# Optimization experiments

Measured on AMD Instinct MI355X. Metric: run time of the kernel, lower is better.

Reference implementation:

```python
import jax, jax.numpy as jnp
import numpy as np

B, T, D, C = 16, 2048, 512, 20
K_EASY, K_HARD = 40, 20
M_BIG, M_SMALL = 7, 3
A4 = A5 = A6 = A7 = 1.0
EPS = 1e-05
DROP_P = 0.6


def setup_inputs() -> dict:
    key = jax.random.key(0)
    ks = jax.random.split(key, 6)
    attn = jax.random.uniform(ks[0], (B, T, 1), dtype=jnp.float32)
    mu = jax.random.normal(ks[1], (B, T, D), dtype=jnp.float32)
    var = jax.random.uniform(ks[2], (B, T, D), dtype=jnp.float32) * 0.9 + 0.1
    mu_clip = jax.random.normal(ks[3], (B, T, D), dtype=jnp.float32)
    text_feat = jax.random.normal(ks[4], (C, D), dtype=jnp.float32)
    keep = (jax.random.uniform(ks[5], (B, T)) >= DROP_P).astype(jnp.float32)
    drop_mask = keep / (1.0 - DROP_P)  # inverted-dropout mask on a ones tensor
    return dict(attn=attn, mu=mu, var=var, mu_clip=mu_clip, text_feat=text_feat, drop_mask=drop_mask)


def _normalize(x, axis=-1):
    n = jnp.linalg.norm(x, axis=axis, keepdims=True)
    return x / jnp.maximum(n, 1e-12)


def _select_topk(scores, emb, k):
    # torch: sort desc, take first k indices, gather along time dim
    _, idx = jax.lax.top_k(scores, k)  # [B,k]
    return jnp.take_along_axis(emb, idx[:, :, None], axis=1)  # [B,k,D]


def _window_reduce(x, w, op_min):
    # binary erosion/dilation along time with structure ones((1,w)), border_value=0
    lo, hi = w // 2, w - 1 - w // 2
    xp = jnp.pad(x, ((0, 0), (lo, hi)), constant_values=0.0)
    if op_min:
        return jax.lax.reduce_window(xp, jnp.inf, jax.lax.min, (1, w), (1, 1), 'VALID')
    return jax.lax.reduce_window(xp, -jnp.inf, jax.lax.max, (1, w), (1, 1), 'VALID')


def _kl_distance(mu_p, cov_p, mu_q, cov_q):
    # vectorized over all (i in k_p) x (j in k_q) pairs
    cov_p = cov_p + EPS
    cov_q = cov_q + EPS
    d = mu_p.shape[-1]
    diff = mu_q[:, None, :, :] - mu_p[:, :, None, :]        # [B,kp,kq,D]
    term1 = 0.5 * jnp.sum(diff * diff / cov_q[:, None, :, :], axis=-1)
    term2 = 0.5 * (jnp.sum(jnp.log(cov_q), -1)[:, None, :] - jnp.sum(jnp.log(cov_p), -1)[:, :, None])
    term3 = 0.5 * jnp.sum(cov_p[:, :, None, :] / cov_q[:, None, :, :], axis=-1)
    dist = term1 + term2 + term3 - 0.5 * d
    return jnp.mean(1.0 / (dist + 1.0), axis=(1, 2))        # [B]


def _prob_contrastive(hard_q, easy_pos, easy_neg):
    pos = _kl_distance(hard_q[0], hard_q[1], easy_pos[0], easy_pos[1])
    neg = _kl_distance(hard_q[0], hard_q[1], easy_neg[0], easy_neg[1])
    return jnp.mean(-(jnp.log(pos) + jnp.log(1.0 - neg)))


def _forward(attn, mu, var, mu_clip, text_feat, drop_mask):
    a = attn[..., 0]                                        # [B,T]
    a_drop = a * drop_mask
    a_rev = jnp.max(a, axis=1, keepdims=True) - a
    a_rev_drop = a_rev * drop_mask
    easy_act = (_select_topk(a_drop, mu, K_EASY), _select_topk(a_drop, var, K_EASY))
    easy_bkg = (_select_topk(a_rev_drop, mu, K_EASY), _select_topk(a_rev_drop, var, K_EASY))

    med = jnp.median(a, axis=1, keepdims=True)
    abin = jnp.where(a > med, 1.0, 0.0)
    er_M = _window_reduce(abin, M_BIG, True)
    er_m = _window_reduce(abin, M_SMALL, True)
    inner = jax.lax.stop_gradient(er_m - er_M)              # mask computed on detached numpy in torch
    dl_m = _window_reduce(abin, M_SMALL, False)
    dl_M = _window_reduce(abin, M_BIG, False)
    outer = jax.lax.stop_gradient(dl_M - dl_m)
    a_inner = a * inner
    a_outer = a * outer
    hard_act = (_select_topk(a_inner, mu, K_HARD), _select_topk(a_inner, var, K_HARD))
    hard_bkg = (_select_topk(a_outer, mu, K_HARD), _select_topk(a_outer, var, K_HARD))

    # Distillation
    sim = jnp.einsum('btd,btd->bt', _normalize(mu), _normalize(mu_clip))
    distill = A4 * (-jnp.log(jnp.mean((sim + 1.0) / 2.0)))

    act_loss = A5 * _prob_contrastive(hard_act, easy_act, easy_bkg)
    bkg_loss = A6 * _prob_contrastive(hard_bkg, easy_bkg, easy_act)

    emb = _normalize(text_feat)
    sim_m = emb @ jax.lax.stop_gradient(emb.T) - jnp.eye(emb.shape[0], dtype=emb.dtype)
    ortho = A7 * jnp.linalg.norm(sim_m)

    total = distill + act_loss + bkg_loss + ortho
    return total, distill, act_loss, bkg_loss, ortho


def reference(attn, mu, var, mu_clip, text_feat, drop_mask):
    return _forward(attn, mu, var, mu_clip, text_feat, drop_mask)
```

## Files before the change

kernel.cpp:

```cpp
#include <hip/hip_runtime.h>
#include <math.h>


#define BB 16
#define TT 2048
#define DD 512
#define CC 20
#define KEASY 40
#define KHARD 20
#define EPSF 1e-5f

typedef unsigned long long u64;

template <int CTRL>
__device__ __forceinline__ float dpp_mov(float x) {
  return __int_as_float(__builtin_amdgcn_update_dpp(
      0, __float_as_int(x), CTRL, 0xF, 0xF, true));
}
template <int CTRL, int RM>
__device__ __forceinline__ unsigned dpp_movu(unsigned x) {
  return (unsigned)__builtin_amdgcn_update_dpp(0, (int)x, CTRL, RM, 0xF, true);
}
__device__ __forceinline__ float wsum63(float v) {
  v += dpp_mov<0x111>(v);
  v += dpp_mov<0x112>(v);
  v += dpp_mov<0x114>(v);
  v += dpp_mov<0x118>(v);
  v += dpp_mov<0x142>(v);
  v += dpp_mov<0x143>(v);
  return v;
}
__device__ __forceinline__ float wsum_bc(float v) {
  return __int_as_float(__builtin_amdgcn_readlane(__float_as_int(wsum63(v)), 63));
}
__device__ __forceinline__ float wmax63(float v) {
  v = fmaxf(v, dpp_mov<0x111>(v));
  v = fmaxf(v, dpp_mov<0x112>(v));
  v = fmaxf(v, dpp_mov<0x114>(v));
  v = fmaxf(v, dpp_mov<0x118>(v));
  v = fmaxf(v, dpp_mov<0x142>(v));
  v = fmaxf(v, dpp_mov<0x143>(v));
  return v;
}
__device__ __forceinline__ unsigned wscanu(unsigned v) {
  v += dpp_movu<0x111, 0xF>(v);
  v += dpp_movu<0x112, 0xF>(v);
  v += dpp_movu<0x114, 0xF>(v);
  v += dpp_movu<0x118, 0xF>(v);
  v += dpp_movu<0x142, 0xa>(v);
  v += dpp_movu<0x143, 0xc>(v);
  return v;
}

__device__ __forceinline__ float radix_kth(const float* sbuf, unsigned k,
                                           unsigned* s_hist4, unsigned* s_state,
                                           int tid, int wid) {
#pragma unroll 1
  for (int round = 0; round < 4; ++round) {
    s_hist4[tid] = 0;
    s_hist4[256 + tid] = 0;
    s_hist4[512 + tid] = 0;
    s_hist4[768 + tid] = 0;
    if (round == 0 && tid == 0) { s_state[0] = 0u; s_state[1] = k; }
    __syncthreads();
    const int shift = 24 - 8 * round;
    const unsigned mask_hi = (round == 0) ? 0u : (0xFFFFFFFFu << (shift + 8));
    const unsigned pref = s_state[0];
    const unsigned kk = s_state[1];
    unsigned* myhist = s_hist4 + (wid << 8);
    unsigned curbin = 0xFFFFFFFFu, curc = 0;
    for (int i = tid; i < TT; i += 256) {
      const unsigned key = __float_as_uint(sbuf[i]);
      if ((key & mask_hi) == pref) {
        const unsigned bin = 255u - ((key >> shift) & 255u);
        if (bin == curbin) {
          curc++;
        } else {
          if (curc) atomicAdd(&myhist[curbin], curc);
          curbin = bin;
          curc = 1;
        }
      }
    }
    if (curc) atomicAdd(&myhist[curbin], curc);
    __syncthreads();
    if (tid < 64) {
      const uint4 h0 = *(const uint4*)(s_hist4 + 4 * tid);
      const uint4 h1 = *(const uint4*)(s_hist4 + 256 + 4 * tid);
      const uint4 h2 = *(const uint4*)(s_hist4 + 512 + 4 * tid);
      const uint4 h3 = *(const uint4*)(s_hist4 + 768 + 4 * tid);
      const unsigned b0 = h0.x + h1.x + h2.x + h3.x;
      const unsigned b1 = h0.y + h1.y + h2.y + h3.y;
      const unsigned b2 = h0.z + h1.z + h2.z + h3.z;
      const unsigned b3 = h0.w + h1.w + h2.w + h3.w;
      const unsigned s0 = b0, s1 = s0 + b1, s2 = s1 + b2, s3 = s2 + b3;
      const unsigned P = wscanu(s3);
      const unsigned E = P - s3;
      const u64 bal = __ballot(P >= kk);
      const int L = (int)__ffsll(bal) - 1;
      if (tid == L) {
        unsigned binj, cb;
        if (E + s0 >= kk)      { binj = 0u; cb = E; }
        else if (E + s1 >= kk) { binj = 1u; cb = E + s0; }
        else if (E + s2 >= kk) { binj = 2u; cb = E + s1; }
        else                   { binj = 3u; cb = E + s2; }
        const unsigned digit = 255u - (4u * (unsigned)tid + binj);
        s_state[0] = pref | (digit << shift);
        s_state[1] = kk - cb;
      }
    }
    __syncthreads();
  }
  return __uint_as_float(s_state[0]);
}

__global__ __launch_bounds__(256, 2) void k_main1(const float* __restrict__ attn,
                                                  const float* __restrict__ drop,
                                                  const float* __restrict__ mu,
                                                  const float* __restrict__ muc,
                                                  const float* __restrict__ var,
                                                  int* __restrict__ idxb,
                                                  float* __restrict__ slogb,
                                                  float* __restrict__ part) {
  const int tid = threadIdx.x, wid = tid >> 6, lane = tid & 63;

  if (blockIdx.x >= 64) {
    __shared__ float s_red[4];
    const int d = blockIdx.x - 64;
    const int row0 = d * 16 + wid * 4;
    const float* pmu = mu + (size_t)row0 * DD + lane * 4;
    const float* pmc = muc + (size_t)row0 * DD + lane * 4;
    float4 x[8], y[8];
#pragma unroll
    for (int r = 0; r < 4; r++) {
      const int off = r * DD;
      x[2 * r]     = *(const float4*)(pmu + off);
      x[2 * r + 1] = *(const float4*)(pmu + off + 256);
      y[2 * r]     = *(const float4*)(pmc + off);
      y[2 * r + 1] = *(const float4*)(pmc + off + 256);
    }
    float wacc = 0.f;
#pragma unroll
    for (int r = 0; r < 4; r++) {
      const float4 cxa = x[2 * r], cxb = x[2 * r + 1];
      const float4 cya = y[2 * r], cyb = y[2 * r + 1];
      float dot = 0.f, n1 = 0.f, n2 = 0.f;
      dot = fmaf(cxa.x, cya.x, fmaf(cxa.y, cya.y, fmaf(cxa.z, cya.z, fmaf(cxa.w, cya.w, dot))));
      n1 = fmaf(cxa.x, cxa.x, fmaf(cxa.y, cxa.y, fmaf(cxa.z, cxa.z, fmaf(cxa.w, cxa.w, n1))));
      n2 = fmaf(cya.x, cya.x, fmaf(cya.y, cya.y, fmaf(cya.z, cya.z, fmaf(cya.w, cya.w, n2))));
      dot = fmaf(cxb.x, cyb.x, fmaf(cxb.y, cyb.y, fmaf(cxb.z, cyb.z, fmaf(cxb.w, cyb.w, dot))));
      n1 = fmaf(cxb.x, cxb.x, fmaf(cxb.y, cxb.y, fmaf(cxb.z, cxb.z, fmaf(cxb.w, cxb.w, n1))));
      n2 = fmaf(cyb.x, cyb.x, fmaf(cyb.y, cyb.y, fmaf(cyb.z, cyb.z, fmaf(cyb.w, cyb.w, n2))));
      dot = wsum63(dot);
      n1 = wsum63(n1);
      n2 = wsum63(n2);
      if (lane == 63) {
        const float sim = dot / (fmaxf(sqrtf(n1), 1e-12f) * fmaxf(sqrtf(n2), 1e-12f));
        wacc += (sim + 1.0f) * 0.5f;
      }
    }
    if (lane == 63) s_red[wid] = wacc;
    __syncthreads();
    if (tid == 0) part[d] = s_red[0] + s_red[1] + s_red[2] + s_red[3];
    return;
  }

  __shared__ float s_a[TT];
  __shared__ float s_v[TT];
  __shared__ __align__(16) unsigned s_hist4[1024];
  __shared__ unsigned s_state[2];
  __shared__ float s_bc[4];
  __shared__ unsigned s_bcu[4];
  __shared__ int s_idx[KEASY];

  const int b = blockIdx.x >> 2, sel = blockIdx.x & 3;
  for (int i = tid; i < TT; i += 256) s_a[i] = attn[b * TT + i];
  __syncthreads();

  float med = 0.f, mx = 0.f;
  if (sel == 1) {
    float lm = 0.f;
    for (int i = tid; i < TT; i += 256) lm = fmaxf(lm, s_a[i]);
    lm = wmax63(lm);
    if (lane == 63) s_bc[wid] = lm;
    __syncthreads();
    mx = fmaxf(fmaxf(s_bc[0], s_bc[1]), fmaxf(s_bc[2], s_bc[3]));
  } else if (sel >= 2) {
    const float v1 = radix_kth(s_a, 1024u, s_hist4, s_state, tid, wid);
    unsigned c = 0;
    float m2 = 0.f;
    for (int i = tid; i < TT; i += 256) {
      const float x = s_a[i];
      c += (x >= v1) ? 1u : 0u;
      m2 = (x < v1) ? fmaxf(m2, x) : m2;
    }
    c = wscanu(c);
    m2 = wmax63(m2);
    if (lane == 63) { s_bc[wid] = m2; s_bcu[wid] = c; }
    __syncthreads();
    const unsigned ctot = s_bcu[0] + s_bcu[1] + s_bcu[2] + s_bcu[3];
    const float m2t = fmaxf(fmaxf(s_bc[0], s_bc[1]), fmaxf(s_bc[2], s_bc[3]));
    const float v2 = (ctot >= 1025u) ? v1 : m2t;
    med = 0.5f * (v1 + v2);
  }

  for (int i = tid; i < TT; i += 256) {
    const float a = s_a[i];
    float score;
    if (sel == 0) {
      score = a * drop[b * TT + i];
    } else if (sel == 1) {
      score = (mx - a) * drop[b * TT + i];
    } else {
      bool sall = true, ball = true, sany = false, bany = false;
#pragma unroll
      for (int o = -3; o <= 3; o++) {
        const int t = i + o;
        const bool one = (t >= 0 && t < TT) ? (s_a[t] > med) : false;
        if (o >= -1 && o <= 1) { sall = sall && one; sany = sany || one; }
        ball = ball && one;
        bany = bany || one;
      }
      score = (sel == 2) ? ((sall && !ball) ? a : 0.f)
                         : ((bany && !sany) ? a : 0.f);
    }
    s_v[i] = score;
  }
  const unsigned K = (sel < 2) ? KEASY : KHARD;
  const float thr = radix_kth(s_v, K, s_hist4, s_state, tid, wid);

  if (tid < 64) {
    float v[32];
#pragma unroll
    for (int r = 0; r < 32; r++) v[r] = s_v[r * 64 + lane];
    unsigned cgt = 0;
#pragma unroll
    for (int r = 0; r < 32; r++) cgt += (unsigned)__popcll(__ballot(v[r] > thr));
    unsigned need = (cgt < K) ? (K - cgt) : 0u;
    unsigned base = 0;
    const u64 lmask = (1ull << lane) - 1;
    int* dst = idxb + sel * (BB * KEASY) + b * KEASY;
#pragma unroll
    for (int r = 0; r < 32; r++) {
      const bool gt = v[r] > thr;
      const bool eq = v[r] == thr;
      const u64 beq = __ballot(eq);
      const unsigned neq = (unsigned)__popcll(beq);
      const unsigned take = (need < neq) ? need : neq;
      const bool tk = eq && ((unsigned)__popcll(beq & lmask) < take);
      const u64 bsel = __ballot(gt || tk);
      if (gt || tk) {
        const unsigned pos = base + (unsigned)__popcll(bsel & lmask);
        if (pos < K) {
          dst[pos] = r * 64 + lane;
          s_idx[pos] = r * 64 + lane;
        }
      }
      base += (unsigned)__popcll(bsel);
      need -= take;
    }
  }
  __syncthreads();

  const int Ksel = (sel < 2) ? KEASY : KHARD;
  for (int j = wid; j < Ksel; j += 4) {
    const int t = s_idx[j];
    const float* row = var + ((size_t)b * TT + t) * DD;
    float a2 = 0.f;
#pragma unroll
    for (int c = 0; c < 2; c++) {
      float4 vv = *(const float4*)(row + c * 256 + lane * 4);
      a2 += __logf(vv.x + EPSF) + __logf(vv.y + EPSF) +
            __logf(vv.z + EPSF) + __logf(vv.w + EPSF);
    }
    a2 = wsum63(a2);
    if (lane == 63) slogb[sel * 640 + b * 40 + j] = a2;
  }
}

__global__ __launch_bounds__(256, 1) void k_part2(const float* __restrict__ mu,
                                                  const float* __restrict__ var,
                                                  const int* __restrict__ idxb,
                                                  const float* __restrict__ slogb,
                                                  const float* __restrict__ text,
                                                  double* __restrict__ acc) {
  __shared__ __align__(16) float smem[2 * KHARD * DD];
  const int tid = threadIdx.x, wid = tid >> 6, lane = tid & 63;
  const int blk = blockIdx.x;

  if (blk < 256) {
    const int b = blk >> 4, klid = (blk >> 2) & 3, qc = blk & 3;
    const int psel = (klid < 2) ? 2 : 3;
    const int qsel = (klid == 0 || klid == 3) ? 0 : 1;
    float* sP1 = smem;
    float* sP2 = smem + KHARD * DD;
    __shared__ float sSlogP[KHARD];
    __shared__ float s_out[4];
    if (tid < KHARD) sSlogP[tid] = slogb[psel * 640 + b * 40 + tid];
    for (int i = tid; i < KHARD * 128; i += 256) {
      const int p = i >> 7, c = (i & 127) * 4;
      const int t = idxb[psel * 640 + b * 40 + p];
      const size_t base = ((size_t)b * TT + t) * DD + c;
      const float4 m = *(const float4*)(mu + base);
      const float4 vv = *(const float4*)(var + base);
      float4 p1;
      p1.x = fmaf(m.x, m.x, vv.x + EPSF);
      p1.y = fmaf(m.y, m.y, vv.y + EPSF);
      p1.z = fmaf(m.z, m.z, vv.z + EPSF);
      p1.w = fmaf(m.w, m.w, vv.w + EPSF);
      *(float4*)(sP1 + p * DD + c) = p1;
      *(float4*)(sP2 + p * DD + c) = m;
    }
    __syncthreads();

    const int d0 = lane * 4, d1 = 256 + lane * 4;
    const int qbase_i = qsel * 640 + b * 40 + qc * 10;
    float wacc = 0.f;
#pragma unroll 1
    for (int j = wid; j < 10; j += 4) {
      const int qidx = idxb[qbase_i + j];
      const float cslq = slogb[qbase_i + j];
      const float* qm = mu + ((size_t)b * TT + qidx) * DD;
      const float* qv = var + ((size_t)b * TT + qidx) * DD;
      const float4 cma = *(const float4*)(qm + d0);
      const float4 cmb = *(const float4*)(qm + d1);
      const float4 cva = *(const float4*)(qv + d0);
      const float4 cvb = *(const float4*)(qv + d1);
      float4 ra, rb, qra, qrb;
      ra.x = 1.0f / (cva.x + EPSF); ra.y = 1.0f / (cva.y + EPSF);
      ra.z = 1.0f / (cva.z + EPSF); ra.w = 1.0f / (cva.w + EPSF);
      rb.x = 1.0f / (cvb.x + EPSF); rb.y = 1.0f / (cvb.y + EPSF);
      rb.z = 1.0f / (cvb.z + EPSF); rb.w = 1.0f / (cvb.w + EPSF);
      qra.x = cma.x * ra.x; qra.y = cma.y * ra.y;
      qra.z = cma.z * ra.z; qra.w = cma.w * ra.w;
      qrb.x = cmb.x * rb.x; qrb.y = cmb.y * rb.y;
      qrb.z = cmb.z * rb.z; qrb.w = cmb.w * rb.w;
      float cqp = cma.x * qra.x + cma.y * qra.y + cma.z * qra.z + cma.w * qra.w +
                  cmb.x * qrb.x + cmb.y * qrb.y + cmb.z * qrb.z + cmb.w * qrb.w;
      const float cq = wsum63(cqp);
      for (int p = 0; p < KHARD; p++) {
        const float4 p1a = *(const float4*)(sP1 + p * DD + d0);
        const float4 p1b = *(const float4*)(sP1 + p * DD + d1);
        const float4 p2a = *(const float4*)(sP2 + p * DD + d0);
        const float4 p2b = *(const float4*)(sP2 + p * DD + d1);
        const float s1 = p1a.x * ra.x + p1a.y * ra.y + p1a.z * ra.z + p1a.w * ra.w +
                         p1b.x * rb.x + p1b.y * rb.y + p1b.z * rb.z + p1b.w * rb.w;
        const float s2 = p2a.x * qra.x + p2a.y * qra.y + p2a.z * qra.z + p2a.w * qra.w +
                         p2b.x * qrb.x + p2b.y * qrb.y + p2b.z * qrb.z + p2b.w * qrb.w;
        const float h = wsum63(fmaf(0.5f, s1, -s2));
        if (lane == 63) {
          const float dist = h + 0.5f * cq + 0.5f * cslq - 0.5f * sSlogP[p] - 256.0f;
          wacc += 1.0f / (dist + 1.0f);
        }
      }
    }
    if (lane == 63) s_out[wid] = wacc;
    __syncthreads();
    if (tid == 0)
      acc[blk] = (double)s_out[0] + s_out[1] + s_out[2] + s_out[3];
    return;
  }

  {
    float* s_e = smem;
    __shared__ float s_red4[4];
    for (int r = wid; r < CC; r += 4) {
      float4 v[2];
      float ss = 0.f;
#pragma unroll
      for (int c = 0; c < 2; c++) {
        v[c] = *(const float4*)(text + r * DD + c * 256 + lane * 4);
        ss += v[c].x * v[c].x + v[c].y * v[c].y + v[c].z * v[c].z + v[c].w * v[c].w;
      }
      ss = wsum_bc(ss);
      const float n = fmaxf(sqrtf(ss), 1e-12f);
#pragma unroll
      for (int c = 0; c < 2; c++) {
        float4 w = v[c];
        w.x /= n; w.y /= n; w.z /= n; w.w /= n;
        *(float4*)(s_e + r * DD + c * 256 + lane * 4) = w;
      }
    }
    __syncthreads();
    float wss = 0.f;
    for (int p = wid; p < CC * CC; p += 4) {
      const int i = p / CC, j = p % CC;
      float dot = 0.f;
#pragma unroll
      for (int c = 0; c < 2; c++) {
        const int d0 = c * 256 + lane * 4;
        const float4 x = *(const float4*)(s_e + i * DD + d0);
        const float4 y = *(const float4*)(s_e + j * DD + d0);
        dot += x.x * y.x + x.y * y.y + x.z * y.z + x.w * y.w;
      }
      dot = wsum63(dot);
      if (lane == 63) {
        const float s = dot - (i == j ? 1.0f : 0.0f);
        wss += s * s;
      }
    }
    if (lane == 63) s_red4[wid] = wss;
    __syncthreads();
    if (tid == 0)
      acc[256] = (double)(s_red4[0] + s_red4[1] + s_red4[2] + s_red4[3]);
  }
}

__global__ __launch_bounds__(256) void k_final(const double* __restrict__ acc,
                                               const float* __restrict__ part,
                                               float* __restrict__ out) {
  __shared__ double sd[256];
  __shared__ double sla[16], slb[16];
  const int tid = threadIdx.x;
  double s = 0.0;
  for (int i = tid; i < 2048; i += 256) s += (double)part[i];
  sd[tid] = s;
  __syncthreads();
  for (int st = 128; st; st >>= 1) {
    if (tid < st) sd[tid] += sd[tid + st];
    __syncthreads();
  }
  if (tid < 16) {
    const double* ab = acc + tid * 16;
    const double pa = (ab[0] + ab[1] + ab[2] + ab[3]) / 800.0;
    const double na = (ab[4] + ab[5] + ab[6] + ab[7]) / 800.0;
    const double pb = (ab[8] + ab[9] + ab[10] + ab[11]) / 800.0;
    const double nb = (ab[12] + ab[13] + ab[14] + ab[15]) / 800.0;
    sla[tid] = -(log(pa) + log(1.0 - na));
    slb[tid] = -(log(pb) + log(1.0 - nb));
  }
  __syncthreads();
  if (tid == 0) {
    double act = 0.0, bkg = 0.0;
    for (int b = 0; b < 16; b++) { act += sla[b]; bkg += slb[b]; }
    act /= 16.0;
    bkg /= 16.0;
    const double distill = -log(sd[0] / (double)(BB * TT));
    const double ortho = sqrt(acc[256]);
    const double total = distill + act + bkg + ortho;
    out[0] = (float)total;
    out[1] = (float)distill;
    out[2] = (float)act;
    out[3] = (float)bkg;
    out[4] = (float)ortho;
  }
}

extern "C" void kernel_launch(void* const* d_in, const int* in_sizes, int n_in,
                              void* d_out, int out_size, void* d_ws, size_t ws_size,
                              hipStream_t stream) {
  const float* attn = (const float*)d_in[0];
  const float* mu   = (const float*)d_in[1];
  const float* var  = (const float*)d_in[2];
  const float* muc  = (const float*)d_in[3];
  const float* text = (const float*)d_in[4];
  const float* drop = (const float*)d_in[5];
  float* out = (float*)d_out;

  double* acc  = (double*)d_ws;
  int* idxb    = (int*)(acc + 257);
  float* slogb = (float*)(idxb + 2560);
  float* part  = (float*)(slogb + 2560);

  k_main1<<<2112, 256, 0, stream>>>(attn, drop, mu, muc, var, idxb, slogb, part);
  k_part2<<<257, 256, 0, stream>>>(mu, var, idxb, slogb, text, acc);
  k_final<<<1, 256, 0, stream>>>(acc, part, out);
}
```

Before: 245.3 us.

## Split distillation into separate grid-strided kernel with register double-buffering

Moves the cosine-similarity distillation pass out of the fused selection kernel into its own 1024-block kernel. Each wave now handles two rows per iteration across four strided iterations and prefetches the next rows into registers while computing the current ones. The selection work becomes a small 64-block kernel. The change aims to improve memory-level parallelism and avoid the heavy shared-memory footprint of the selection blocks limiting occupancy for the bandwidth-bound distill blocks, at the cost of an extra launch and the loss of concurrent overlap between selection and distillation within one grid.

After: 255.1 us. 1.04x slower.

```diff
diff --git a/kernel.cpp b/kernel.cpp
--- a/kernel.cpp
+++ b/kernel.cpp
@@ -114,57 +114,12 @@
   return __uint_as_float(s_state[0]);
 }
 
-__global__ __launch_bounds__(256, 2) void k_main1(const float* __restrict__ attn,
-                                                  const float* __restrict__ drop,
-                                                  const float* __restrict__ mu,
-                                                  const float* __restrict__ muc,
-                                                  const float* __restrict__ var,
-                                                  int* __restrict__ idxb,
-                                                  float* __restrict__ slogb,
-                                                  float* __restrict__ part) {
+__global__ __launch_bounds__(256, 2) void k_sel(const float* __restrict__ attn,
+                                                const float* __restrict__ drop,
+                                                const float* __restrict__ var,
+                                                int* __restrict__ idxb,
+                                                float* __restrict__ slogb) {
   const int tid = threadIdx.x, wid = tid >> 6, lane = tid & 63;
-
-  if (blockIdx.x >= 64) {
-    __shared__ float s_red[4];
-    const int d = blockIdx.x - 64;
-    const int row0 = d * 16 + wid * 4;
-    const float* pmu = mu + (size_t)row0 * DD + lane * 4;
-    const float* pmc = muc + (size_t)row0 * DD + lane * 4;
-    float4 x[8], y[8];
-#pragma unroll
-    for (int r = 0; r < 4; r++) {
-      const int off = r * DD;
-      x[2 * r]     = *(const float4*)(pmu + off);
-      x[2 * r + 1] = *(const float4*)(pmu + off + 256);
-      y[2 * r]     = *(const float4*)(pmc + off);
-      y[2 * r + 1] = *(const float4*)(pmc + off + 256);
-    }
-    float wacc = 0.f;
-#pragma unroll
-    for (int r = 0; r < 4; r++) {
-      const float4 cxa = x[2 * r], cxb = x[2 * r + 1];
-      const float4 cya = y[2 * r], cyb = y[2 * r + 1];
-      float dot = 0.f, n1 = 0.f, n2 = 0.f;
-      dot = fmaf(cxa.x, cya.x, fmaf(cxa.y, cya.y, fmaf(cxa.z, cya.z, fmaf(cxa.w, cya.w, dot))));
-      n1 = fmaf(cxa.x, cxa.x, fmaf(cxa.y, cxa.y, fmaf(cxa.z, cxa.z, fmaf(cxa.w, cxa.w, n1))));
-      n2 = fmaf(cya.x, cya.x, fmaf(cya.y, cya.y, fmaf(cya.z, cya.z, fmaf(cya.w, cya.w, n2))));
-      dot = fmaf(cxb.x, cyb.x, fmaf(cxb.y, cyb.y, fmaf(cxb.z, cyb.z, fmaf(cxb.w, cyb.w, dot))));
-      n1 = fmaf(cxb.x, cxb.x, fmaf(cxb.y, cxb.y, fmaf(cxb.z, cxb.z, fmaf(cxb.w, cxb.w, n1))));
-      n2 = fmaf(cyb.x, cyb.x, fmaf(cyb.y, cyb.y, fmaf(cyb.z, cyb.z, fmaf(cyb.w, cyb.w, n2))));
-      dot = wsum63(dot);
-      n1 = wsum63(n1);
-      n2 = wsum63(n2);
-      if (lane == 63) {
-        const float sim = dot / (fmaxf(sqrtf(n1), 1e-12f) * fmaxf(sqrtf(n2), 1e-12f));
-        wacc += (sim + 1.0f) * 0.5f;
-      }
-    }
-    if (lane == 63) s_red[wid] = wacc;
-    __syncthreads();
-    if (tid == 0) part[d] = s_red[0] + s_red[1] + s_red[2] + s_red[3];
-    return;
-  }
-
   __shared__ float s_a[TT];
   __shared__ float s_v[TT];
   __shared__ __align__(16) unsigned s_hist4[1024];
@@ -276,6 +231,69 @@
     a2 = wsum63(a2);
     if (lane == 63) slogb[sel * 640 + b * 40 + j] = a2;
   }
+}
+
+__device__ __forceinline__ float rowsim(const float4 cxa, const float4 cxb,
+                                        const float4 cya, const float4 cyb) {
+  float dot = 0.f, n1 = 0.f, n2 = 0.f;
+  dot = fmaf(cxa.x, cya.x, fmaf(cxa.y, cya.y, fmaf(cxa.z, cya.z, fmaf(cxa.w, cya.w, dot))));
+  n1 = fmaf(cxa.x, cxa.x, fmaf(cxa.y, cxa.y, fmaf(cxa.z, cxa.z, fmaf(cxa.w, cxa.w, n1))));
+  n2 = fmaf(cya.x, cya.x, fmaf(cya.y, cya.y, fmaf(cya.z, cya.z, fmaf(cya.w, cya.w, n2))));
+  dot = fmaf(cxb.x, cyb.x, fmaf(cxb.y, cyb.y, fmaf(cxb.z, cyb.z, fmaf(cxb.w, cyb.w, dot))));
+  n1 = fmaf(cxb.x, cxb.x, fmaf(cxb.y, cxb.y, fmaf(cxb.z, cxb.z, fmaf(cxb.w, cxb.w, n1))));
+  n2 = fmaf(cyb.x, cyb.x, fmaf(cyb.y, cyb.y, fmaf(cyb.z, cyb.z, fmaf(cyb.w, cyb.w, n2))));
+  dot = wsum63(dot);
+  n1 = wsum63(n1);
+  n2 = wsum63(n2);
+  return dot / (fmaxf(sqrtf(n1), 1e-12f) * fmaxf(sqrtf(n2), 1e-12f));
+}
+
+__global__ __launch_bounds__(256, 2) void k_dist(const float* __restrict__ mu,
+                                                 const float* __restrict__ muc,
+                                                 float* __restrict__ part) {
+  __shared__ float s_red[4];
+  const int tid = threadIdx.x, wid = tid >> 6, lane = tid & 63;
+  const int w = (int)blockIdx.x * 4 + wid;
+  const int d0 = lane * 4;
+  size_t off = (size_t)w * (2 * DD);
+  const size_t stride = (size_t)4096 * (2 * DD);
+
+  float4 xc0 = *(const float4*)(mu + off + d0);
+  float4 xc1 = *(const float4*)(mu + off + d0 + 256);
+  float4 xc2 = *(const float4*)(mu + off + DD + d0);
+  float4 xc3 = *(const float4*)(mu + off + DD + d0 + 256);
+  float4 yc0 = *(const float4*)(muc + off + d0);
+  float4 yc1 = *(const float4*)(muc + off + d0 + 256);
+  float4 yc2 = *(const float4*)(muc + off + DD + d0);
+  float4 yc3 = *(const float4*)(muc + off + DD + d0 + 256);
+
+  float wacc = 0.f;
+#pragma unroll
+  for (int it = 0; it < 4; ++it) {
+    float4 xn0, xn1, xn2, xn3, yn0, yn1, yn2, yn3;
+    if (it < 3) {
+      const size_t o2 = off + stride;
+      xn0 = *(const float4*)(mu + o2 + d0);
+      xn1 = *(const float4*)(mu + o2 + d0 + 256);
+      xn2 = *(const float4*)(mu + o2 + DD + d0);
+      xn3 = *(const float4*)(mu + o2 + DD + d0 + 256);
+      yn0 = *(const float4*)(muc + o2 + d0);
+      yn1 = *(const float4*)(muc + o2 + d0 + 256);
+      yn2 = *(const float4*)(muc + o2 + DD + d0);
+      yn3 = *(const float4*)(muc + o2 + DD + d0 + 256);
+    }
+    const float sim0 = rowsim(xc0, xc1, yc0, yc1);
+    const float sim1 = rowsim(xc2, xc3, yc2, yc3);
+    if (lane == 63) wacc += (sim0 + 1.0f) * 0.5f + (sim1 + 1.0f) * 0.5f;
+    if (it < 3) {
+      xc0 = xn0; xc1 = xn1; xc2 = xn2; xc3 = xn3;
+      yc0 = yn0; yc1 = yn1; yc2 = yn2; yc3 = yn3;
+      off += stride;
+    }
+  }
+  if (lane == 63) s_red[wid] = wacc;
+  __syncthreads();
+  if (tid == 0) part[blockIdx.x] = s_red[0] + s_red[1] + s_red[2] + s_red[3];
 }
 
 __global__ __launch_bounds__(256, 1) void k_part2(const float* __restrict__ mu,
@@ -413,7 +431,7 @@
   __shared__ double sla[16], slb[16];
   const int tid = threadIdx.x;
   double s = 0.0;
-  for (int i = tid; i < 2048; i += 256) s += (double)part[i];
+  for (int i = tid; i < 1024; i += 256) s += (double)part[i];
   sd[tid] = s;
   __syncthreads();
   for (int st = 128; st; st >>= 1) {
@@ -462,7 +480,8 @@
   float* slogb = (float*)(idxb + 2560);
   float* part  = (float*)(slogb + 2560);
 
-  k_main1<<<2112, 256, 0, stream>>>(attn, drop, mu, muc, var, idxb, slogb, part);
+  k_sel<<<64, 256, 0, stream>>>(attn, drop, var, idxb, slogb);
+  k_dist<<<1024, 256, 0, stream>>>(mu, muc, part);
   k_part2<<<257, 256, 0, stream>>>(mu, var, idxb, slogb, text, acc);
   k_final<<<1, 256, 0, stream>>>(acc, part, out);
 }
```
